# Kernel optimization log

Measured on AMD Instinct MI355X. Metric: run time of the kernel, lower is better.

## Reference

```python
import jax, jax.numpy as jnp
import numpy as np

N = 50000    # total nodes
F = 32       # raw feature dim
DEG = 32     # padded neighbors per node per relation
B = 2048     # batch nodes
R = 3        # relations


def setup_inputs() -> dict:
    key = jax.random.key(0)
    ks = jax.random.split(key, 12)
    return {
        "nodes": jax.random.randint(ks[0], (B,), 0, N, dtype=jnp.int32),
        "feat_data": jax.random.normal(ks[1], (N, F), dtype=jnp.float32),
        "adj": jax.random.randint(ks[2], (R, N, DEG), 0, N, dtype=jnp.int32),
        "prior": jax.random.uniform(ks[3], (2,), minval=0.1, maxval=0.9, dtype=jnp.float32),
        "w_mlp": jax.random.normal(ks[4], (F, 64), dtype=jnp.float32) * 0.1,
        "b_mlp": jnp.zeros((64,), jnp.float32),
        "alpha1": jax.random.normal(ks[5], (128, R), dtype=jnp.float32) * 0.1,
        "alpha2": jax.random.normal(ks[6], (256, R), dtype=jnp.float32) * 0.1,
        "w_d2": jax.random.normal(ks[7], (448, 2), dtype=jnp.float32) * 0.05,
        "b_d2": jnp.zeros((2,), jnp.float32),
        "w_d1": jax.random.normal(ks[8], (2, 1), dtype=jnp.float32) * 0.5,
        "b_d1": jnp.zeros((1,), jnp.float32),
    }


def _inter_agg(h_all, adj, nodes, alpha, embed_dim):
    """One InterAgg layer. h_all: (N, D) previous-layer features for all nodes;
    adj: (R, N, deg) neighbor ids; nodes: (B,) batch ids; alpha: (2E, R).
    Returns (B, D + 2E)."""
    emb = h_all[:, -embed_dim:]                      # (N, E) last-E slice as in original
    self_full = jnp.take(h_all, nodes, axis=0)       # (B, D)
    self_emb = self_full[:, -embed_dim:]             # (B, E)
    feats = []
    for r in range(R):  # small fixed relation count
        neigh = jnp.take(adj[r], nodes, axis=0)      # (B, deg)
        gathered = jnp.take(emb, neigh.reshape(-1), axis=0)
        agg = gathered.reshape(neigh.shape[0], neigh.shape[1], embed_dim).mean(axis=1)  # masked-mean
        feats.append(jnp.concatenate([agg, self_emb - agg], axis=1))  # IntraAgg concat
    stack = jnp.stack(feats)                         # (R, B, 2E)
    W = jax.nn.softmax(alpha, axis=1)                # (2E, R)
    inter = jnp.einsum('rbe,er->be', stack, W)       # weighted relation combine
    return jnp.concatenate([self_full, inter], axis=1)


def reference(nodes, feat_data, adj, prior, w_mlp, b_mlp, alpha1, alpha2, w_d2, b_d2, w_d1, b_d1):
    # MLP over all nodes (union set == all nodes; per-node values identical)
    h0 = jax.nn.relu(feat_data @ w_mlp + b_mlp)      # (N, 64)
    all_nodes = jnp.arange(h0.shape[0], dtype=jnp.int32)
    h1 = _inter_agg(h0, adj, all_nodes, alpha1, 64)  # (N, 192)
    h2 = _inter_agg(h1, adj, nodes, alpha2, 128)     # (B, 448)
    x = h2 @ w_d2 + b_d2                             # Dense(2)
    x = jax.nn.leaky_relu(x, negative_slope=0.3)
    x = x + jnp.log(prior)
    return jax.nn.sigmoid(x @ w_d1 + b_d1)           # (B, 1)
```

## Files before the change

kernel.cpp:

```cpp
#include <hip/hip_runtime.h>
#include <hip/hip_fp16.h>
#include <math.h>

#define N_NODES 50000
#define F_IN 32
#define DEG 32
#define BATCH 2048
#define NB_STRIDE 100

typedef _Float16 half8 __attribute__((ext_vector_type(8)));
typedef _Float16 half2v __attribute__((ext_vector_type(2)));
typedef int int4v __attribute__((ext_vector_type(4)));
typedef unsigned int uint2v __attribute__((ext_vector_type(2)));
typedef float f32x2 __attribute__((ext_vector_type(2)));

__device__ __forceinline__ void softmax3(float a0, float a1, float a2,
                                         float& w0, float& w1, float& w2) {
    float m = fmaxf(a0, fmaxf(a1, a2));
    float e0 = __expf(a0 - m), e1 = __expf(a1 - m), e2 = __expf(a2 - m);
    float s = 1.f / (e0 + e1 + e2);
    w0 = e0 * s; w1 = e1 * s; w2 = e2 * s;
}

__device__ __forceinline__ f32x2 shfl_xor_f2(f32x2 v, int m) {
    v.x = __shfl_xor(v.x, m, 64);
    v.y = __shfl_xor(v.y, m, 64);
    return v;
}

__global__ __launch_bounds__(256) void mlp_kernel(
        const float* __restrict__ feat,
        const float* __restrict__ w,
        const float* __restrict__ b,
        const float* __restrict__ alpha1,
        const float* __restrict__ alpha2,
        float* __restrict__ sw1,
        float* __restrict__ sw2,
        _Float16* __restrict__ h0h,
        unsigned char* __restrict__ h0q) {
    __shared__ float wl[F_IN * 64];
    __shared__ float fl[8 * F_IN];
    int tid = threadIdx.x;
    if (blockIdx.x == 0) {
        for (int q = tid; q < 384; q += 256) {
            const float* src = (q < 128) ? (alpha1 + q * 3) : (alpha2 + (q - 128) * 3);
            float* dst = (q < 128) ? (sw1 + q * 3) : (sw2 + (q - 128) * 3);
            float w0, w1, w2;
            softmax3(src[0], src[1], src[2], w0, w1, w2);
            dst[0] = w0; dst[1] = w1; dst[2] = w2;
        }
    }
    for (int i = tid; i < F_IN * 64; i += 256) wl[i] = w[i];
    int local = tid >> 5;
    int f2 = (tid & 31) * 2;
    float b0 = b[f2], b1 = b[f2 + 1];
    const int noct = N_NODES / 8;
    for (int q = blockIdx.x; q < noct; q += gridDim.x) {
        int n0 = q * 8;
        __syncthreads();
        fl[tid] = __builtin_nontemporal_load(feat + (size_t)n0 * F_IN + tid);
        __syncthreads();
        float a0 = b0, a1 = b1;
#pragma unroll
        for (int k = 0; k < F_IN; ++k) {
            float v = fl[local * F_IN + k];
            a0 = fmaf(v, wl[k * 64 + f2], a0);
            a1 = fmaf(v, wl[k * 64 + f2 + 1], a1);
        }
        a0 = fmaxf(a0, 0.f);
        a1 = fmaxf(a1, 0.f);
        int n = n0 + local;
        half2v hv = {(_Float16)a0, (_Float16)a1};
        *reinterpret_cast<half2v*>(h0h + (size_t)n * 64 + f2) = hv;
        unsigned pk = __builtin_amdgcn_cvt_pk_fp8_f32(a0, a1, 0u, false);
        *reinterpret_cast<unsigned short*>(h0q + (size_t)n * 64 + f2) =
            (unsigned short)pk;
    }
}

__global__ __launch_bounds__(128) void layer1_kernel(
        const int* __restrict__ adj,
        const unsigned char* __restrict__ h0q,
        const _Float16* __restrict__ h0h,
        const float* __restrict__ sw1,
        _Float16* __restrict__ i1h,
        unsigned char* __restrict__ i1q) {
    __shared__ int nb[16 * NB_STRIDE];
    __shared__ float swl[384];
    int tid = threadIdx.x;
    int n0 = blockIdx.x * 16;
    if (tid < 96)
        reinterpret_cast<float4*>(swl)[tid] = reinterpret_cast<const float4*>(sw1)[tid];
#pragma unroll
    for (int q = tid; q < 384; q += 128) {
        int r = q >> 7;
        int idx = q & 127;
        int m = idx >> 3;
        int d4 = (idx & 7) * 4;
        int4v v = __builtin_nontemporal_load(reinterpret_cast<const int4v*>(
                adj + ((size_t)r * N_NODES + (n0 + m)) * DEG + d4));
        *reinterpret_cast<int4v*>(&nb[m * NB_STRIDE + r * 32 + d4]) = v;
    }
    __syncthreads();
    int w = tid >> 6, j = tid & 63;
    int m = w * 8 + (j >> 3);
    int e = j & 7;
    int n = n0 + m;
    const int* nbrow = nb + m * NB_STRIDE;
    const unsigned char* qb = h0q + 8 * e;
    f32x2 acc0[4] = {}, acc1[4] = {}, acc2[4] = {};
#pragma unroll 8
    for (int t = 0; t < 32; ++t) {
        uint2v d = *reinterpret_cast<const uint2v*>(qb + (size_t)((unsigned)nbrow[t] * 64u));
        acc0[0] += __builtin_amdgcn_cvt_pk_f32_fp8(d.x, false);
        acc0[1] += __builtin_amdgcn_cvt_pk_f32_fp8(d.x, true);
        acc0[2] += __builtin_amdgcn_cvt_pk_f32_fp8(d.y, false);
        acc0[3] += __builtin_amdgcn_cvt_pk_f32_fp8(d.y, true);
    }
#pragma unroll 8
    for (int t = 32; t < 64; ++t) {
        uint2v d = *reinterpret_cast<const uint2v*>(qb + (size_t)((unsigned)nbrow[t] * 64u));
        acc1[0] += __builtin_amdgcn_cvt_pk_f32_fp8(d.x, false);
        acc1[1] += __builtin_amdgcn_cvt_pk_f32_fp8(d.x, true);
        acc1[2] += __builtin_amdgcn_cvt_pk_f32_fp8(d.y, false);
        acc1[3] += __builtin_amdgcn_cvt_pk_f32_fp8(d.y, true);
    }
#pragma unroll 8
    for (int t = 64; t < 96; ++t) {
        uint2v d = *reinterpret_cast<const uint2v*>(qb + (size_t)((unsigned)nbrow[t] * 64u));
        acc2[0] += __builtin_amdgcn_cvt_pk_f32_fp8(d.x, false);
        acc2[1] += __builtin_amdgcn_cvt_pk_f32_fp8(d.x, true);
        acc2[2] += __builtin_amdgcn_cvt_pk_f32_fp8(d.y, false);
        acc2[3] += __builtin_amdgcn_cvt_pk_f32_fp8(d.y, true);
    }

    half8 sv = *reinterpret_cast<const half8*>(h0h + (size_t)n * 64 + 8 * e);
    float wA[24], wB[24];
    {
        const float4* pa = reinterpret_cast<const float4*>(swl + 24 * e);
        const float4* pb = reinterpret_cast<const float4*>(swl + 192 + 24 * e);
#pragma unroll
        for (int q = 0; q < 6; ++q) {
            float4 ta = pa[q], tb = pb[q];
            wA[4 * q] = ta.x; wA[4 * q + 1] = ta.y; wA[4 * q + 2] = ta.z; wA[4 * q + 3] = ta.w;
            wB[4 * q] = tb.x; wB[4 * q + 1] = tb.y; wB[4 * q + 2] = tb.z; wB[4 * q + 3] = tb.w;
        }
    }
    const float inv = 1.f / 32.f;
    float oa[8], ob[8];
    half8 ra, rb;
#pragma unroll
    for (int i = 0; i < 8; ++i) {
        float a0 = acc0[i >> 1][i & 1] * inv;
        float a1 = acc1[i >> 1][i & 1] * inv;
        float a2 = acc2[i >> 1][i & 1] * inv;
        float s = (float)sv[i];
        oa[i] = wA[3 * i] * a0 + wA[3 * i + 1] * a1 + wA[3 * i + 2] * a2;
        ob[i] = wB[3 * i] * (s - a0) + wB[3 * i + 1] * (s - a1) + wB[3 * i + 2] * (s - a2);
        ra[i] = (_Float16)oa[i];
        rb[i] = (_Float16)ob[i];
    }
    __builtin_nontemporal_store(__builtin_bit_cast(int4v, ra),
        reinterpret_cast<int4v*>(i1h + (size_t)n * 128 + 8 * e));
    __builtin_nontemporal_store(__builtin_bit_cast(int4v, rb),
        reinterpret_cast<int4v*>(i1h + (size_t)n * 128 + 64 + 8 * e));
    unsigned qa0 = __builtin_amdgcn_cvt_pk_fp8_f32(oa[0], oa[1], 0u, false);
    qa0 = __builtin_amdgcn_cvt_pk_fp8_f32(oa[2], oa[3], qa0, true);
    unsigned qa1 = __builtin_amdgcn_cvt_pk_fp8_f32(oa[4], oa[5], 0u, false);
    qa1 = __builtin_amdgcn_cvt_pk_fp8_f32(oa[6], oa[7], qa1, true);
    uint2v ua = {qa0, qa1};
    __builtin_nontemporal_store(ua,
        reinterpret_cast<uint2v*>(i1q + (size_t)n * 128 + 8 * e));
    unsigned qb0 = __builtin_amdgcn_cvt_pk_fp8_f32(ob[0], ob[1], 0u, false);
    qb0 = __builtin_amdgcn_cvt_pk_fp8_f32(ob[2], ob[3], qb0, true);
    unsigned qb1 = __builtin_amdgcn_cvt_pk_fp8_f32(ob[4], ob[5], 0u, false);
    qb1 = __builtin_amdgcn_cvt_pk_fp8_f32(ob[6], ob[7], qb1, true);
    uint2v ub = {qb0, qb1};
    __builtin_nontemporal_store(ub,
        reinterpret_cast<uint2v*>(i1q + (size_t)n * 128 + 64 + 8 * e));
}

__global__ __launch_bounds__(64) void layer2_kernel(
        const int* __restrict__ nodes,
        const int* __restrict__ adj,
        const _Float16* __restrict__ h0h,
        const _Float16* __restrict__ i1h,
        const unsigned char* __restrict__ i1q,
        const float* __restrict__ sw2,
        const float* __restrict__ w_d2,
        const float* __restrict__ b_d2,
        const float* __restrict__ w_d1,
        const float* __restrict__ b_d1,
        const float* __restrict__ prior,
        float* __restrict__ out) {
    __shared__ int nb[96];
    __shared__ float swl[768];
    int tid = threadIdx.x;
    int bb = blockIdx.x;
    int n = nodes[bb];
#pragma unroll
    for (int q = tid; q < 192; q += 64)
        reinterpret_cast<float4*>(swl)[q] = reinterpret_cast<const float4*>(sw2)[q];
    if (tid < 24) {
        int r = tid >> 3, d4 = (tid & 7) * 4;
        int4v v = __builtin_nontemporal_load(reinterpret_cast<const int4v*>(
                adj + ((size_t)r * N_NODES + n) * DEG + d4));
        *reinterpret_cast<int4v*>(&nb[r * 32 + d4]) = v;
    }
    __syncthreads();
    int j = tid;
    int g = j >> 4, e = j & 15;
    int idxs[24];
#pragma unroll
    for (int t = 0; t < 24; ++t) idxs[t] = nb[t * 4 + g];
    const unsigned char* qbase = i1q + 8 * e;
    f32x2 acc0[4] = {}, acc1[4] = {}, acc2[4] = {};
#pragma unroll
    for (int t = 0; t < 8; ++t) {
        uint2v d = *reinterpret_cast<const uint2v*>(
            qbase + (size_t)((unsigned)idxs[t] * 128u));
        acc0[0] += __builtin_amdgcn_cvt_pk_f32_fp8(d.x, false);
        acc0[1] += __builtin_amdgcn_cvt_pk_f32_fp8(d.x, true);
        acc0[2] += __builtin_amdgcn_cvt_pk_f32_fp8(d.y, false);
        acc0[3] += __builtin_amdgcn_cvt_pk_f32_fp8(d.y, true);
    }
#pragma unroll
    for (int t = 8; t < 16; ++t) {
        uint2v d = *reinterpret_cast<const uint2v*>(
            qbase + (size_t)((unsigned)idxs[t] * 128u));
        acc1[0] += __builtin_amdgcn_cvt_pk_f32_fp8(d.x, false);
        acc1[1] += __builtin_amdgcn_cvt_pk_f32_fp8(d.x, true);
        acc1[2] += __builtin_amdgcn_cvt_pk_f32_fp8(d.y, false);
        acc1[3] += __builtin_amdgcn_cvt_pk_f32_fp8(d.y, true);
    }
#pragma unroll
    for (int t = 16; t < 24; ++t) {
        uint2v d = *reinterpret_cast<const uint2v*>(
            qbase + (size_t)((unsigned)idxs[t] * 128u));
        acc2[0] += __builtin_amdgcn_cvt_pk_f32_fp8(d.x, false);
        acc2[1] += __builtin_amdgcn_cvt_pk_f32_fp8(d.x, true);
        acc2[2] += __builtin_amdgcn_cvt_pk_f32_fp8(d.y, false);
        acc2[3] += __builtin_amdgcn_cvt_pk_f32_fp8(d.y, true);
    }
#pragma unroll
    for (int mm = 16; mm <= 32; mm <<= 1) {
#pragma unroll
        for (int q = 0; q < 4; ++q) {
            acc0[q] += shfl_xor_f2(acc0[q], mm);
            acc1[q] += shfl_xor_f2(acc1[q], mm);
            acc2[q] += shfl_xor_f2(acc2[q], mm);
        }
    }
    const float inv = 1.f / 32.f;
    float p0 = 0.f, p1 = 0.f;
    if (g == 0) {
        half8 sv = *reinterpret_cast<const half8*>(i1h + (size_t)n * 128 + 8 * e);
        const float* wa = swl + 24 * e;
        const float* wb = swl + 384 + 24 * e;
#pragma unroll
        for (int i = 0; i < 8; ++i) {
            int f = 8 * e + i;
            float a0 = acc0[i >> 1][i & 1] * inv;
            float a1 = acc1[i >> 1][i & 1] * inv;
            float a2 = acc2[i >> 1][i & 1] * inv;
            float s = (float)sv[i];
            float i2a = wa[3 * i] * a0 + wa[3 * i + 1] * a1 + wa[3 * i + 2] * a2;
            float i2b = wb[3 * i] * (s - a0) + wb[3 * i + 1] * (s - a1) +
                        wb[3 * i + 2] * (s - a2);
            p0 += i2a * w_d2[(192 + f) * 2 + 0] + i2b * w_d2[(320 + f) * 2 + 0];
            p1 += i2a * w_d2[(192 + f) * 2 + 1] + i2b * w_d2[(320 + f) * 2 + 1];
        }
    } else if (g == 1) {
#pragma unroll
        for (int i = 0; i < 4; ++i) {
            int f = 4 * e + i;
            float s = (float)h0h[(size_t)n * 64 + f];
            p0 += s * w_d2[f * 2 + 0];
            p1 += s * w_d2[f * 2 + 1];
        }
    } else if (g == 2) {
        half8 sv = *reinterpret_cast<const half8*>(i1h + (size_t)n * 128 + 8 * e);
#pragma unroll
        for (int i = 0; i < 8; ++i) {
            int f = 8 * e + i;
            float s = (float)sv[i];
            p0 += s * w_d2[(64 + f) * 2 + 0];
            p1 += s * w_d2[(64 + f) * 2 + 1];
        }
    }
#pragma unroll
    for (int mm = 1; mm <= 32; mm <<= 1) {
        p0 += __shfl_xor(p0, mm, 64);
        p1 += __shfl_xor(p1, mm, 64);
    }
    if (j == 0) {
        float x0 = p0 + b_d2[0], x1 = p1 + b_d2[1];
        x0 = x0 > 0.f ? x0 : 0.3f * x0;
        x1 = x1 > 0.f ? x1 : 0.3f * x1;
        x0 += __logf(prior[0]);
        x1 += __logf(prior[1]);
        float z = x0 * w_d1[0] + x1 * w_d1[1] + b_d1[0];
        out[bb] = 1.f / (1.f + __expf(-z));
    }
}

extern "C" void kernel_launch(void* const* d_in, const int* in_sizes, int n_in,
                              void* d_out, int out_size, void* d_ws, size_t ws_size,
                              hipStream_t stream) {
    const int*   nodes  = (const int*)d_in[0];
    const float* feat   = (const float*)d_in[1];
    const int*   adj    = (const int*)d_in[2];
    const float* prior  = (const float*)d_in[3];
    const float* w_mlp  = (const float*)d_in[4];
    const float* b_mlp  = (const float*)d_in[5];
    const float* alpha1 = (const float*)d_in[6];
    const float* alpha2 = (const float*)d_in[7];
    const float* w_d2   = (const float*)d_in[8];
    const float* b_d2   = (const float*)d_in[9];
    const float* w_d1   = (const float*)d_in[10];
    const float* b_d1   = (const float*)d_in[11];
    float* out = (float*)d_out;

    float* sw1 = (float*)d_ws;
    float* sw2 = sw1 + 128 * 3;
    _Float16* h0h = (_Float16*)((char*)d_ws + 8192);
    _Float16* i1h = h0h + (size_t)N_NODES * 64;
    unsigned char* h0q = (unsigned char*)(i1h + (size_t)N_NODES * 128);
    unsigned char* i1q = h0q + (size_t)N_NODES * 64;

    mlp_kernel<<<2048, 256, 0, stream>>>(feat, w_mlp, b_mlp, alpha1, alpha2,
                                         sw1, sw2, h0h, h0q);
    layer1_kernel<<<N_NODES / 16, 128, 0, stream>>>(adj, h0q, h0h, sw1, i1h, i1q);
    layer2_kernel<<<BATCH, 64, 0, stream>>>(nodes, adj, h0h, i1h, i1q, sw2,
                                            w_d2, b_d2, w_d1, b_d1, prior, out);
}
```

Baseline: 59.05 us.

## Drop fp16 copies of intermediates, read self features from fp8, batch layer2

Removes the fp16 copies of h0 and the layer-1 output. Every kernel now keeps only the fp8 arrays and reads self features from them, which cuts global write and read traffic in the MLP and layer1 kernels. Layer2 now processes four batch nodes per 256-thread block instead of one per 64-thread block, sharing the softmax weight load and cutting block count. The cost is lower precision for self features and the dense inputs, since fp8 replaces fp16, which may affect accuracy tolerance.

```diff
diff --git a/kernel.cpp b/kernel.cpp
--- a/kernel.cpp
+++ b/kernel.cpp
@@ -8,8 +8,6 @@
 #define BATCH 2048
 #define NB_STRIDE 100
 
-typedef _Float16 half8 __attribute__((ext_vector_type(8)));
-typedef _Float16 half2v __attribute__((ext_vector_type(2)));
 typedef int int4v __attribute__((ext_vector_type(4)));
 typedef unsigned int uint2v __attribute__((ext_vector_type(2)));
 typedef float f32x2 __attribute__((ext_vector_type(2)));
@@ -36,7 +34,6 @@
         const float* __restrict__ alpha2,
         float* __restrict__ sw1,
         float* __restrict__ sw2,
-        _Float16* __restrict__ h0h,
         unsigned char* __restrict__ h0q) {
     __shared__ float wl[F_IN * 64];
     __shared__ float fl[8 * F_IN];
@@ -70,8 +67,6 @@
         a0 = fmaxf(a0, 0.f);
         a1 = fmaxf(a1, 0.f);
         int n = n0 + local;
-        half2v hv = {(_Float16)a0, (_Float16)a1};
-        *reinterpret_cast<half2v*>(h0h + (size_t)n * 64 + f2) = hv;
         unsigned pk = __builtin_amdgcn_cvt_pk_fp8_f32(a0, a1, 0u, false);
         *reinterpret_cast<unsigned short*>(h0q + (size_t)n * 64 + f2) =
             (unsigned short)pk;
@@ -81,9 +76,7 @@
 __global__ __launch_bounds__(128) void layer1_kernel(
         const int* __restrict__ adj,
         const unsigned char* __restrict__ h0q,
-        const _Float16* __restrict__ h0h,
         const float* __restrict__ sw1,
-        _Float16* __restrict__ i1h,
         unsigned char* __restrict__ i1q) {
     __shared__ int nb[16 * NB_STRIDE];
     __shared__ float swl[384];
@@ -134,7 +127,16 @@
         acc2[3] += __builtin_amdgcn_cvt_pk_f32_fp8(d.y, true);
     }
 
-    half8 sv = *reinterpret_cast<const half8*>(h0h + (size_t)n * 64 + 8 * e);
+    float sarr[8];
+    {
+        uint2v sd = *reinterpret_cast<const uint2v*>(qb + (size_t)((unsigned)n * 64u));
+        f32x2 s0 = __builtin_amdgcn_cvt_pk_f32_fp8(sd.x, false);
+        f32x2 s1 = __builtin_amdgcn_cvt_pk_f32_fp8(sd.x, true);
+        f32x2 s2 = __builtin_amdgcn_cvt_pk_f32_fp8(sd.y, false);
+        f32x2 s3 = __builtin_amdgcn_cvt_pk_f32_fp8(sd.y, true);
+        sarr[0] = s0.x; sarr[1] = s0.y; sarr[2] = s1.x; sarr[3] = s1.y;
+        sarr[4] = s2.x; sarr[5] = s2.y; sarr[6] = s3.x; sarr[7] = s3.y;
+    }
     float wA[24], wB[24];
     {
         const float4* pa = reinterpret_cast<const float4*>(swl + 24 * e);
@@ -148,22 +150,15 @@
     }
     const float inv = 1.f / 32.f;
     float oa[8], ob[8];
-    half8 ra, rb;
 #pragma unroll
     for (int i = 0; i < 8; ++i) {
         float a0 = acc0[i >> 1][i & 1] * inv;
         float a1 = acc1[i >> 1][i & 1] * inv;
         float a2 = acc2[i >> 1][i & 1] * inv;
-        float s = (float)sv[i];
+        float s = sarr[i];
         oa[i] = wA[3 * i] * a0 + wA[3 * i + 1] * a1 + wA[3 * i + 2] * a2;
         ob[i] = wB[3 * i] * (s - a0) + wB[3 * i + 1] * (s - a1) + wB[3 * i + 2] * (s - a2);
-        ra[i] = (_Float16)oa[i];
-        rb[i] = (_Float16)ob[i];
-    }
-    __builtin_nontemporal_store(__builtin_bit_cast(int4v, ra),
-        reinterpret_cast<int4v*>(i1h + (size_t)n * 128 + 8 * e));
-    __builtin_nontemporal_store(__builtin_bit_cast(int4v, rb),
-        reinterpret_cast<int4v*>(i1h + (size_t)n * 128 + 64 + 8 * e));
+    }
     unsigned qa0 = __builtin_amdgcn_cvt_pk_fp8_f32(oa[0], oa[1], 0u, false);
     qa0 = __builtin_amdgcn_cvt_pk_fp8_f32(oa[2], oa[3], qa0, true);
     unsigned qa1 = __builtin_amdgcn_cvt_pk_fp8_f32(oa[4], oa[5], 0u, false);
@@ -180,11 +175,10 @@
         reinterpret_cast<uint2v*>(i1q + (size_t)n * 128 + 64 + 8 * e));
 }
 
-__global__ __launch_bounds__(64) void layer2_kernel(
+__global__ __launch_bounds__(256) void layer2_kernel(
         const int* __restrict__ nodes,
         const int* __restrict__ adj,
-        const _Float16* __restrict__ h0h,
-        const _Float16* __restrict__ i1h,
+        const unsigned char* __restrict__ h0q,
         const unsigned char* __restrict__ i1q,
         const float* __restrict__ sw2,
         const float* __restrict__ w_d2,
@@ -193,26 +187,32 @@
         const float* __restrict__ b_d1,
         const float* __restrict__ prior,
         float* __restrict__ out) {
-    __shared__ int nb[96];
+    __shared__ int nb[4][96];
+    __shared__ int nid[4];
     __shared__ float swl[768];
     int tid = threadIdx.x;
-    int bb = blockIdx.x;
-    int n = nodes[bb];
-#pragma unroll
-    for (int q = tid; q < 192; q += 64)
+    int b0 = blockIdx.x * 4;
+    if (tid < 4) nid[tid] = nodes[b0 + tid];
+    if (tid >= 64 && tid < 256) {
+        int q = tid - 64;
         reinterpret_cast<float4*>(swl)[q] = reinterpret_cast<const float4*>(sw2)[q];
-    if (tid < 24) {
-        int r = tid >> 3, d4 = (tid & 7) * 4;
+    }
+    __syncthreads();
+    if (tid < 96) {
+        int local = tid / 24, rem = tid - local * 24;
+        int r = rem >> 3, d4 = (rem & 7) * 4;
         int4v v = __builtin_nontemporal_load(reinterpret_cast<const int4v*>(
-                adj + ((size_t)r * N_NODES + n) * DEG + d4));
-        *reinterpret_cast<int4v*>(&nb[r * 32 + d4]) = v;
+                adj + ((size_t)r * N_NODES + nid[local]) * DEG + d4));
+        *reinterpret_cast<int4v*>(&nb[local][r * 32 + d4]) = v;
     }
     __syncthreads();
-    int j = tid;
+    int local = tid >> 6, j = tid & 63;
+    int bb = b0 + local;
+    int n = nid[local];
     int g = j >> 4, e = j & 15;
     int idxs[24];
 #pragma unroll
-    for (int t = 0; t < 24; ++t) idxs[t] = nb[t * 4 + g];
+    for (int t = 0; t < 24; ++t) idxs[t] = nb[local][t * 4 + g];
     const unsigned char* qbase = i1q + 8 * e;
     f32x2 acc0[4] = {}, acc1[4] = {}, acc2[4] = {};
 #pragma unroll
@@ -254,7 +254,17 @@
     const float inv = 1.f / 32.f;
     float p0 = 0.f, p1 = 0.f;
     if (g == 0) {
-        half8 sv = *reinterpret_cast<const half8*>(i1h + (size_t)n * 128 + 8 * e);
+        float sarr[8];
+        {
+            uint2v sd = *reinterpret_cast<const uint2v*>(
+                qbase + (size_t)((unsigned)n * 128u));
+            f32x2 s0 = __builtin_amdgcn_cvt_pk_f32_fp8(sd.x, false);
+            f32x2 s1 = __builtin_amdgcn_cvt_pk_f32_fp8(sd.x, true);
+            f32x2 s2 = __builtin_amdgcn_cvt_pk_f32_fp8(sd.y, false);
+            f32x2 s3 = __builtin_amdgcn_cvt_pk_f32_fp8(sd.y, true);
+            sarr[0] = s0.x; sarr[1] = s0.y; sarr[2] = s1.x; sarr[3] = s1.y;
+            sarr[4] = s2.x; sarr[5] = s2.y; sarr[6] = s3.x; sarr[7] = s3.y;
+        }
         const float* wa = swl + 24 * e;
         const float* wb = swl + 384 + 24 * e;
 #pragma unroll
@@ -263,7 +273,7 @@
             float a0 = acc0[i >> 1][i & 1] * inv;
             float a1 = acc1[i >> 1][i & 1] * inv;
             float a2 = acc2[i >> 1][i & 1] * inv;
-            float s = (float)sv[i];
+            float s = sarr[i];
             float i2a = wa[3 * i] * a0 + wa[3 * i + 1] * a1 + wa[3 * i + 2] * a2;
             float i2b = wb[3 * i] * (s - a0) + wb[3 * i + 1] * (s - a1) +
                         wb[3 * i + 2] * (s - a2);
@@ -271,21 +281,33 @@
             p1 += i2a * w_d2[(192 + f) * 2 + 1] + i2b * w_d2[(320 + f) * 2 + 1];
         }
     } else if (g == 1) {
+        unsigned d = *reinterpret_cast<const unsigned*>(h0q + (size_t)n * 64 + 4 * e);
+        f32x2 lo = __builtin_amdgcn_cvt_pk_f32_fp8(d, false);
+        f32x2 hi = __builtin_amdgcn_cvt_pk_f32_fp8(d, true);
+        float sv[4] = {lo.x, lo.y, hi.x, hi.y};
 #pragma unroll
         for (int i = 0; i < 4; ++i) {
             int f = 4 * e + i;
-            float s = (float)h0h[(size_t)n * 64 + f];
-            p0 += s * w_d2[f * 2 + 0];
-            p1 += s * w_d2[f * 2 + 1];
+            p0 += sv[i] * w_d2[f * 2 + 0];
+            p1 += sv[i] * w_d2[f * 2 + 1];
         }
     } else if (g == 2) {
-        half8 sv = *reinterpret_cast<const half8*>(i1h + (size_t)n * 128 + 8 * e);
+        float sarr[8];
+        {
+            uint2v sd = *reinterpret_cast<const uint2v*>(
+                qbase + (size_t)((unsigned)n * 128u));
+            f32x2 s0 = __builtin_amdgcn_cvt_pk_f32_fp8(sd.x, false);
+            f32x2 s1 = __builtin_amdgcn_cvt_pk_f32_fp8(sd.x, true);
+            f32x2 s2 = __builtin_amdgcn_cvt_pk_f32_fp8(sd.y, false);
+            f32x2 s3 = __builtin_amdgcn_cvt_pk_f32_fp8(sd.y, true);
+            sarr[0] = s0.x; sarr[1] = s0.y; sarr[2] = s1.x; sarr[3] = s1.y;
+            sarr[4] = s2.x; sarr[5] = s2.y; sarr[6] = s3.x; sarr[7] = s3.y;
+        }
 #pragma unroll
         for (int i = 0; i < 8; ++i) {
             int f = 8 * e + i;
-            float s = (float)sv[i];
-            p0 += s * w_d2[(64 + f) * 2 + 0];
-            p1 += s * w_d2[(64 + f) * 2 + 1];
+            p0 += sarr[i] * w_d2[(64 + f) * 2 + 0];
+            p1 += sarr[i] * w_d2[(64 + f) * 2 + 1];
         }
     }
 #pragma unroll
@@ -323,14 +345,12 @@
 
     float* sw1 = (float*)d_ws;
     float* sw2 = sw1 + 128 * 3;
-    _Float16* h0h = (_Float16*)((char*)d_ws + 8192);
-    _Float16* i1h = h0h + (size_t)N_NODES * 64;
-    unsigned char* h0q = (unsigned char*)(i1h + (size_t)N_NODES * 128);
+    unsigned char* h0q = (unsigned char*)((char*)d_ws + 8192);
     unsigned char* i1q = h0q + (size_t)N_NODES * 64;
 
     mlp_kernel<<<2048, 256, 0, stream>>>(feat, w_mlp, b_mlp, alpha1, alpha2,
-                                         sw1, sw2, h0h, h0q);
-    layer1_kernel<<<N_NODES / 16, 128, 0, stream>>>(adj, h0q, h0h, sw1, i1h, i1q);
-    layer2_kernel<<<BATCH, 64, 0, stream>>>(nodes, adj, h0h, i1h, i1q, sw2,
-                                            w_d2, b_d2, w_d1, b_d1, prior, out);
-}
+                                         sw1, sw2, h0q);
+    layer1_kernel<<<N_NODES / 16, 128, 0, stream>>>(adj, h0q, sw1, i1q);
+    layer2_kernel<<<BATCH / 4, 256, 0, stream>>>(nodes, adj, h0q, i1q, sw2,
+                                                 w_d2, b_d2, w_d1, b_d1, prior, out);
+}
```

Measured after the change: 55.26 us, median of 2. 1.07x faster.
